# Optimization experiments

Hardware: AMD Instinct MI355X
Metric: run time of the kernel (lower is better)

## Reference

```python
import jax, jax.numpy as jnp
import numpy as np

N = 20000      # nodes / tokens
H = 256        # hidden_size
NH = 8         # num_heads
HD = NH * H    # num_heads * hidden_size = 2048
EPS = 1e-5


def setup_inputs() -> dict:
    key = jax.random.key(0)
    ks = jax.random.split(key, 24)

    def lin_w(k, i, o):
        # xavier-ish scale for a Linear weight stored as [in, out]
        return jax.random.normal(k, (i, o), jnp.float32) * (1.0 / np.sqrt(i))

    inp = {
        'q': jax.random.normal(ks[0], (N, H), jnp.float32),
        'k': jax.random.normal(ks[1], (N, H), jnp.float32),
        'v': jax.random.normal(ks[2], (N, H), jnp.float32),
        'layer': 1,
        'Wq1': lin_w(ks[3], H, HD), 'bq1': jnp.zeros((HD,), jnp.float32),
        'Wk1': lin_w(ks[4], H, HD), 'bk1': jnp.zeros((HD,), jnp.float32),
        'Wq2': lin_w(ks[5], H, HD), 'bq2': jnp.zeros((HD,), jnp.float32),
        'Wk2': lin_w(ks[6], H, HD), 'bk2': jnp.zeros((HD,), jnp.float32),
        'Wv':  lin_w(ks[7], H, HD), 'bv':  jnp.zeros((HD,), jnp.float32),
        'ln_g': jnp.ones((HD,), jnp.float32),
        'ln_b': jnp.zeros((HD,), jnp.float32),
        'Wo': lin_w(ks[8], HD, H), 'bo': jnp.zeros((H,), jnp.float32),
        'lq1': jax.random.normal(ks[9], (H,), jnp.float32) * 0.1,
        'lk1': jax.random.normal(ks[10], (H,), jnp.float32) * 0.1,
        'lq2': jax.random.normal(ks[11], (H,), jnp.float32) * 0.1,
        'lk2': jax.random.normal(ks[12], (H,), jnp.float32) * 0.1,
    }
    return inp


def reference(q, k, v, layer, Wq1, bq1, Wk1, bk1, Wq2, bq2, Wk2, bk2,
              Wv, bv, ln_g, ln_b, Wo, bo, lq1, lk1, lq2, lk2):
    # projections: [N, H] -> [N, HD]
    q1 = q @ Wq1 + bq1
    k1 = k @ Wk1 + bk1
    q2 = q @ Wq2 + bq2
    k2 = k @ Wk2 + bk2
    vv = v @ Wv + bv

    # linear attention: K^T V -> [HD, HD]  (dropout is identity in eval mode)
    k1v = k1.T @ vv
    k2v = k2.T @ vv

    # lambda gating (scalars)
    lam1 = jnp.exp(jnp.sum(lq1 * lk1))
    lam2 = jnp.exp(jnp.sum(lq2 * lk2))
    lam_init = 0.8 - 0.6 * jnp.exp(jnp.asarray(-0.3 * layer, jnp.float32))
    lam_full = lam1 - lam2 + lam_init

    # Q @ (K^T V), differential subtraction: [N, HD]
    x = q1 @ k1v - lam_full * (q2 @ k2v)

    # LayerNorm over last dim (biased variance, eps=1e-5, like torch)
    mu = jnp.mean(x, axis=-1, keepdims=True)
    var = jnp.mean(jnp.square(x - mu), axis=-1, keepdims=True)
    x = (x - mu) / jnp.sqrt(var + EPS) * ln_g + ln_b

    x = x * (1.0 - lam_init)
    return x @ Wo + bo  # [N, H]
```

## Files before the change

kernel.cpp:

```cpp
#include <hip/hip_runtime.h>
#include <stdint.h>

typedef __bf16 bf16x8 __attribute__((ext_vector_type(8)));
typedef __bf16 bf16x4v __attribute__((ext_vector_type(4)));
typedef float f32x4 __attribute__((ext_vector_type(4)));
typedef float f32x2 __attribute__((ext_vector_type(2)));
typedef unsigned short u16x4 __attribute__((ext_vector_type(4)));
typedef unsigned short u16x8 __attribute__((ext_vector_type(8)));

#define NTOK 20000
#define HIW  256
#define HD   2048
#define LDK  66
#define BUFS 8448

static __device__ __forceinline__ float bf2f(unsigned short h) {
  union { unsigned u; float f; } c; c.u = ((unsigned)h) << 16;
  return c.f;
}
static __device__ __forceinline__ unsigned short fbits(float x) {
  __bf16 h = (__bf16)x;
  return __builtin_bit_cast(unsigned short, h);
}

#define WRED(x) { x += __shfl_xor(x,32); x += __shfl_xor(x,16); x += __shfl_xor(x,8); \
                  x += __shfl_xor(x,4);  x += __shfl_xor(x,2);  x += __shfl_xor(x,1); }


__global__ __launch_bounds__(512) void k_front(
    const float* __restrict__ kk, const float* __restrict__ vv,
    const float* __restrict__ Wq1, const float* __restrict__ Wk1,
    const float* __restrict__ Wq2, const float* __restrict__ Wk2,
    const float* __restrict__ lq1, const float* __restrict__ lk1,
    const float* __restrict__ lq2, const float* __restrict__ lk2,
    const float* __restrict__ bq1, const float* __restrict__ bk1,
    const float* __restrict__ bq2, const float* __restrict__ bk2,
    const int* __restrict__ layer,
    unsigned short* __restrict__ S_part, float* __restrict__ skp, float* __restrict__ svp,
    unsigned short* __restrict__ Pc_part, float* __restrict__ scal) {
  __shared__ unsigned short SH[4 * BUFS];
  const int b = blockIdx.x;
  const int t = threadIdx.x, lane = t & 63, wave = t >> 6;
  const int wr = (wave >> 1) * 32, wc = (wave & 1) * 64;
  const int r15 = lane & 15, kg = (lane >> 4) * 8;

  if (b < 256) {
    const int z = b & 63, by = (b >> 6) & 1, bx = (b >> 7) & 1;
    const int i0 = bx * 128, j0 = by * 128;
    const int n_lo = z * 313;
    const int cnt = (NTOK - n_lo < 313) ? (NTOK - n_lo) : 313;
    f32x4 acc[2][4];
    #pragma unroll
    for (int m = 0; m < 2; ++m)
      #pragma unroll
      for (int n = 0; n < 4; ++n) acc[m][n] = (f32x4){0.f, 0.f, 0.f, 0.f};

    const int matsel = t >> 8, col = t & 127, half = (t >> 7) & 1;
    const float* src = matsel ? vv : kk;
    const int gcol = (matsel ? j0 : i0) + col;
    unsigned short* Lb0 = SH + matsel * BUFS;
    const int tbase = half * 32;
    float csum = 0.f;
    float rA[32], rB[32];

#define LOADK(dst, KT)                                                        \
    { _Pragma("unroll")                                                       \
      for (int g = 0; g < 32; ++g) {                                          \
        int nn = (KT) * 64 + tbase + g;                                       \
        dst[g] = (nn < cnt) ? src[(size_t)(n_lo + nn) * HIW + gcol] : 0.f;    \
      } }
#define WRITEK(dstp, rr)                                                      \
    { _Pragma("unroll")                                                       \
      for (int g4 = 0; g4 < 8; ++g4) {                                        \
        bf16x4v o;                                                            \
        _Pragma("unroll")                                                     \
        for (int u = 0; u < 4; ++u) {                                         \
          float x = rr[g4 * 4 + u]; csum += x; o[u] = (__bf16)x;              \
        }                                                                     \
        *(bf16x4v*)&dstp[col * LDK + tbase + g4 * 4] = o;                     \
      } }

    LOADK(rA, 0)
    WRITEK(Lb0, rA)
    LOADK(rB, 1)
    asm volatile("s_waitcnt lgkmcnt(0)" ::: "memory");
    __builtin_amdgcn_s_barrier();

    #pragma unroll
    for (int kt = 0; kt < 5; ++kt) {
      const unsigned short* Akr = SH + (kt & 1) * 2 * BUFS;
      const unsigned short* Bkr = Akr + BUFS;
      __builtin_amdgcn_s_setprio(1);
      #pragma unroll
      for (int ks = 0; ks < 2; ++ks) {
        const int ko = ks * 32 + kg;
        bf16x8 ah[2], bh[4];
        #pragma unroll
        for (int m = 0; m < 2; ++m)
          ah[m] = *(const bf16x8*)&Akr[(wr + m * 16 + r15) * LDK + ko];
        #pragma unroll
        for (int n = 0; n < 4; ++n)
          bh[n] = *(const bf16x8*)&Bkr[(wc + n * 16 + r15) * LDK + ko];
        #pragma unroll
        for (int m = 0; m < 2; ++m)
          #pragma unroll
          for (int n = 0; n < 4; ++n)
            acc[m][n] = __builtin_amdgcn_mfma_f32_16x16x32_bf16(ah[m], bh[n], acc[m][n], 0, 0, 0);
      }
      __builtin_amdgcn_s_setprio(0);
      if (kt < 4) {
        unsigned short* Ld = SH + ((kt + 1) & 1) * 2 * BUFS + matsel * BUFS;
        if ((kt & 1) == 0) {
          WRITEK(Ld, rB)
          if (kt + 2 <= 4) LOADK(rA, kt + 2)
        } else {
          WRITEK(Ld, rA)
          if (kt + 2 <= 4) LOADK(rB, kt + 2)
        }
      }
      asm volatile("s_waitcnt lgkmcnt(0)" ::: "memory");
      __builtin_amdgcn_s_barrier();
    }
#undef LOADK
#undef WRITEK
    const int rg = (lane >> 4) * 4;
    unsigned short* Sp = S_part + (size_t)z * 65536;
    #pragma unroll
    for (int m = 0; m < 2; ++m)
      #pragma unroll
      for (int n = 0; n < 4; ++n)
        #pragma unroll
        for (int r = 0; r < 4; ++r)
          Sp[(i0 + wr + m * 16 + rg + r) * 256 + (j0 + wc + n * 16 + r15)] = fbits(acc[m][n][r]);
    if (bx == by) {
      float* red = (float*)SH;
      red[t] = csum;
      __syncthreads();
      if (t < 128)      skp[z * 256 + i0 + t]         = red[t] + red[t + 128];
      else if (t < 256) svp[z * 256 + j0 + (t - 128)] = red[t + 128] + red[t + 256];
    }
  } else if (b < 384) {
    const int idx = b - 256;
    const int pair = idx >> 6, rem = idx & 63;
    const int z = rem & 15, by = (rem >> 4) & 1, bx = (rem >> 5) & 1;
    const int i0 = bx * 128, j0 = by * 128;
    const float* Wa = pair ? Wq2 : Wq1;
    const float* Wb = pair ? Wk2 : Wk1;
    f32x4 acc[2][4];
    #pragma unroll
    for (int m = 0; m < 2; ++m)
      #pragma unroll
      for (int n = 0; n < 4; ++n) acc[m][n] = (f32x4){0.f, 0.f, 0.f, 0.f};
    unsigned short* Ak = SH;
    unsigned short* Bk = SH + BUFS;
    const int srow = t >> 2, sq = (t & 3) * 16;
    for (int kt = 0; kt < 2; ++kt) {
      const int kb = z * 128 + kt * 64 + sq;
      __syncthreads();
      #pragma unroll
      for (int c = 0; c < 4; ++c) {
        f32x4 a = *(const f32x4*)&Wa[(size_t)(i0 + srow) * HD + kb + c * 4];
        f32x4 bb = *(const f32x4*)&Wb[(size_t)(j0 + srow) * HD + kb + c * 4];
        bf16x4v oa, ob;
        #pragma unroll
        for (int u = 0; u < 4; ++u) { oa[u] = (__bf16)a[u]; ob[u] = (__bf16)bb[u]; }
        *(bf16x4v*)&Ak[srow * LDK + sq + c * 4] = oa;
        *(bf16x4v*)&Bk[srow * LDK + sq + c * 4] = ob;
      }
      __syncthreads();
      __builtin_amdgcn_s_setprio(1);
      #pragma unroll
      for (int ks = 0; ks < 2; ++ks) {
        const int ko = ks * 32 + kg;
        bf16x8 ah[2], bh[4];
        #pragma unroll
        for (int m = 0; m < 2; ++m)
          ah[m] = *(const bf16x8*)&Ak[(wr + m * 16 + r15) * LDK + ko];
        #pragma unroll
        for (int n = 0; n < 4; ++n)
          bh[n] = *(const bf16x8*)&Bk[(wc + n * 16 + r15) * LDK + ko];
        #pragma unroll
        for (int m = 0; m < 2; ++m)
          #pragma unroll
          for (int n = 0; n < 4; ++n)
            acc[m][n] = __builtin_amdgcn_mfma_f32_16x16x32_bf16(ah[m], bh[n], acc[m][n], 0, 0, 0);
      }
      __builtin_amdgcn_s_setprio(0);
    }
    const int rg = (lane >> 4) * 4;
    unsigned short* Pp = Pc_part + (size_t)(pair * 16 + z) * 65536;
    #pragma unroll
    for (int m = 0; m < 2; ++m)
      #pragma unroll
      for (int n = 0; n < 4; ++n)
        #pragma unroll
        for (int r = 0; r < 4; ++r)
          Pp[(i0 + wr + m * 16 + rg + r) * 256 + (j0 + wc + n * 16 + r15)] = fbits(acc[m][n][r]);
  } else {
    float* red = (float*)SH;
    if (t < 256) {
      float p1 = lq1[t] * lk1[t], p2 = lq2[t] * lk2[t];
      float d1 = 0.f, d2 = 0.f;
      #pragma unroll
      for (int u = 0; u < 8; ++u) {
        d1 += bq1[t * 8 + u] * bk1[t * 8 + u];
        d2 += bq2[t * 8 + u] * bk2[t * 8 + u];
      }
      WRED(p1); WRED(p2); WRED(d1); WRED(d2);
      int w = t >> 6;
      if ((t & 63) == 0) { red[w] = p1; red[4 + w] = p2; red[8 + w] = d1; red[12 + w] = d2; }
    }
    __syncthreads();
    if (t == 0) {
      float s1 = red[0] + red[1] + red[2] + red[3];
      float s2 = red[4] + red[5] + red[6] + red[7];
      float dd1 = red[8] + red[9] + red[10] + red[11];
      float dd2 = red[12] + red[13] + red[14] + red[15];
      float li = 0.8f - 0.6f * expf(-0.3f * (float)layer[0]);
      float lam = expf(s1) - expf(s2) + li;
      scal[0] = lam; scal[1] = -lam; scal[2] = 1.0f - li; scal[3] = li;
      scal[4] = dd1 - lam * dd2;
    }
  }
}

__global__ __launch_bounds__(256) void k_sred(
    const unsigned short* __restrict__ S_part, const unsigned short* __restrict__ Pc_part,
    const float* __restrict__ skp, const float* __restrict__ svp,
    float* __restrict__ S, float* __restrict__ Pc,
    float* __restrict__ sk, float* __restrict__ sv,
    const float* __restrict__ Wk1, const float* __restrict__ Wk2,
    const float* __restrict__ Wq1, const float* __restrict__ Wq2,
    const float* __restrict__ bq1, const float* __restrict__ bq2,
    const float* __restrict__ bk1, const float* __restrict__ bk2,
    const float* __restrict__ scal, float* __restrict__ gc, float* __restrict__ uc) {
  int b = blockIdx.x, t = threadIdx.x;
  if (b < 64) {
    size_t idx = (size_t)b * 1024 + t * 4;
    f32x4 s = {0.f, 0.f, 0.f, 0.f};
    #pragma unroll 4
    for (int z = 0; z < 64; ++z) {
      u16x4 h = *(const u16x4*)&S_part[(size_t)z * 65536 + idx];
      #pragma unroll
      for (int u = 0; u < 4; ++u) s[u] += bf2f(h[u]);
    }
    *(f32x4*)&S[idx] = s;
  } else if (b < 96) {
    size_t idx = (size_t)(b - 64) * 2048 + t * 8;
    float s1[8] = {}, s2[8] = {};
    #pragma unroll 2
    for (int z = 0; z < 16; ++z) {
      u16x8 ha = *(const u16x8*)&Pc_part[(size_t)z * 65536 + idx];
      u16x8 hb = *(const u16x8*)&Pc_part[(size_t)(16 + z) * 65536 + idx];
      #pragma unroll
      for (int u = 0; u < 8; ++u) { s1[u] += bf2f(ha[u]); s2[u] += bf2f(hb[u]); }
    }
    float lam = scal[0];
    #pragma unroll
    for (int u = 0; u < 8; ++u) Pc[idx + u] = s1[u] - lam * s2[u];
  } else if (b < 98) {
    const float* src = (b == 96) ? skp : svp;
    float s = 0.f;
    for (int z = 0; z < 64; ++z) s += src[z * 256 + t];
    if (b == 96) sk[t] = s; else sv[t] = s;
  } else {
    int bb = b - 98, lane = t & 63, w = t >> 6;
    bool dogc = bb < 16;
    const float* A1 = dogc ? Wk1 : Wq1;
    const float* A2 = dogc ? Wk2 : Wq2;
    const float* x1 = dogc ? bq1 : bk1;
    const float* x2 = dogc ? bq2 : bk2;
    float* outv = dogc ? gc : uc;
    float lam = scal[0];
    int rb = (bb & 15) * 16 + w * 4;
    for (int q2 = 0; q2 < 4; ++q2) {
      int row = rb + q2;
      float s1 = 0.f, s2 = 0.f;
      #pragma unroll
      for (int c = 0; c < 8; ++c) {
        int kk2 = c * 256 + lane * 4;
        f32x4 a1 = *(const f32x4*)&A1[(size_t)row * HD + kk2];
        f32x4 a2 = *(const f32x4*)&A2[(size_t)row * HD + kk2];
        f32x4 v1 = *(const f32x4*)&x1[kk2];
        f32x4 v2 = *(const f32x4*)&x2[kk2];
        #pragma unroll
        for (int u = 0; u < 4; ++u) { s1 += a1[u] * v1[u]; s2 += a2[u] * v2[u]; }
      }
      WRED(s1); WRED(s2);
      if (lane == 0) outv[row] = s1 - lam * s2;
    }
  }
}

__global__ __launch_bounds__(256) void k_ac(
    const float* __restrict__ Pc, const float* __restrict__ S,
    const float* __restrict__ gc, const float* __restrict__ sk,
    float* __restrict__ Ac, float* __restrict__ tc, float* __restrict__ rv,
    float* __restrict__ scal) {
  int b = blockIdx.x, t = threadIdx.x;
  if (b < 32) {
    __shared__ float Pt[32][68];
    __shared__ float St[64][68];
    int i0 = (b >> 2) * 32, j0 = (b & 3) * 64;
    int ti = t >> 5, tj = t & 31;
    float acc[4][2] = {};
    for (int kt = 0; kt < 256; kt += 64) {
      __syncthreads();
      {
        int rr = t >> 3, c8 = (t & 7) * 8;
        *(f32x4*)&Pt[rr][c8] = *(const f32x4*)&Pc[(i0 + rr) * 256 + kt + c8];
        *(f32x4*)&Pt[rr][c8 + 4] = *(const f32x4*)&Pc[(i0 + rr) * 256 + kt + c8 + 4];
      }
      {
        int rr = t >> 2, c16 = (t & 3) * 16;
        #pragma unroll
        for (int c = 0; c < 4; ++c)
          *(f32x4*)&St[rr][c16 + c * 4] = *(const f32x4*)&S[(kt + rr) * 256 + j0 + c16 + c * 4];
      }
      __syncthreads();
      #pragma unroll 8
      for (int k2 = 0; k2 < 64; ++k2) {
        float a[4];
        #pragma unroll
        for (int u = 0; u < 4; ++u) a[u] = Pt[ti * 4 + u][k2];
        f32x2 b2 = *(const f32x2*)&St[k2][tj * 2];
        #pragma unroll
        for (int u = 0; u < 4; ++u) { acc[u][0] += a[u] * b2[0]; acc[u][1] += a[u] * b2[1]; }
      }
    }
    #pragma unroll
    for (int u = 0; u < 4; ++u) {
      Ac[(i0 + ti * 4 + u) * 256 + j0 + tj * 2] = acc[u][0];
      Ac[(i0 + ti * 4 + u) * 256 + j0 + tj * 2 + 1] = acc[u][1];
    }
  } else if (b == 32) {
    int lane = t & 63, w = t >> 6;
    f32x4 sk4 = *(const f32x4*)&sk[lane * 4];
    for (int ii = 0; ii < 64; ++ii) {
      int i = w * 64 + ii;
      f32x4 p4 = *(const f32x4*)&Pc[i * 256 + lane * 4];
      float s = p4[0] * sk4[0] + p4[1] * sk4[1] + p4[2] * sk4[2] + p4[3] * sk4[3];
      WRED(s);
      if (lane == 0) tc[i] = s;
    }
  } else {
    float s0 = 0.f, s1 = 0.f, s2 = 0.f, s3 = 0.f;
    #pragma unroll 4
    for (int i = 0; i < 256; i += 4) {
      s0 += gc[i] * S[i * 256 + t];
      s1 += gc[i + 1] * S[(i + 1) * 256 + t];
      s2 += gc[i + 2] * S[(i + 2) * 256 + t];
      s3 += gc[i + 3] * S[(i + 3) * 256 + t];
    }
    rv[t] = (s0 + s1) + (s2 + s3);
    if (t < 64) {
      f32x4 g4 = *(const f32x4*)&gc[t * 4];
      f32x4 sk4 = *(const f32x4*)&sk[t * 4];
      float a = g4[0] * sk4[0] + g4[1] * sk4[1] + g4[2] * sk4[2] + g4[3] * sk4[3];
      WRED(a);
      if (t == 0) scal[5] = a;
    }
  }
}

__global__ __launch_bounds__(256) void k_gc(
    const float* __restrict__ Ac, const float* __restrict__ Wv,
    const float* __restrict__ tc, const float* __restrict__ uc,
    const float* __restrict__ sv, const float* __restrict__ rv,
    const float* __restrict__ bv, const float* __restrict__ scal,
    float* __restrict__ Gc, float* __restrict__ cc) {
  __shared__ float At[64][68];
  __shared__ float Bt[64][132];
  __shared__ float svr[256], rvr[256];
  int t = threadIdx.x;
  int i0 = blockIdx.x * 64, j0 = blockIdx.y * 128;
  int ti = t >> 5, tj = t & 31;
  svr[t] = sv[t]; rvr[t] = rv[t];
  float acc[8][4] = {};
  f32x4 swa = {0.f, 0.f, 0.f, 0.f}, sca = {0.f, 0.f, 0.f, 0.f};
  for (int kt = 0; kt < 256; kt += 64) {
    __syncthreads();
    {
      int rr = t >> 2, c16 = (t & 3) * 16;
      #pragma unroll
      for (int c = 0; c < 4; ++c)
        *(f32x4*)&At[rr][c16 + c * 4] = *(const f32x4*)&Ac[(i0 + rr) * 256 + kt + c16 + c * 4];
    }
    {
      int rr = t >> 2, c32 = (t & 3) * 32;
      #pragma unroll
      for (int c = 0; c < 8; ++c)
        *(f32x4*)&Bt[rr][c32 + c * 4] = *(const f32x4*)&Wv[(size_t)(kt + rr) * HD + j0 + c32 + c * 4];
    }
    __syncthreads();
    #pragma unroll 8
    for (int k2 = 0; k2 < 64; ++k2) {
      float a[8];
      #pragma unroll
      for (int u = 0; u < 8; ++u) a[u] = At[ti * 8 + u][k2];
      f32x4 b = *(const f32x4*)&Bt[k2][tj * 4];
      float svk = svr[kt + k2], rvk = rvr[kt + k2];
      swa += b * svk; sca += b * rvk;
      #pragma unroll
      for (int u = 0; u < 8; ++u)
        #pragma unroll
        for (int v = 0; v < 4; ++v) acc[u][v] += a[u] * b[v];
    }
  }
  int j = j0 + tj * 4;
  f32x4 bv4 = *(const f32x4*)&bv[j];
  f32x4 wnb;
  #pragma unroll
  for (int v = 0; v < 4; ++v) wnb[v] = swa[v] + 20000.0f * bv4[v];
  if (blockIdx.x == 0 && ti == 0) {
    float ac = scal[5], dc = scal[4];
    f32x4 ccv;
    #pragma unroll
    for (int v = 0; v < 4; ++v) ccv[v] = sca[v] + ac * bv4[v] + dc * wnb[v];
    *(f32x4*)&cc[j] = ccv;
  }
  #pragma unroll
  for (int u = 0; u < 8; ++u) {
    int i = i0 + ti * 8 + u;
    float tci = tc[i], uci = uc[i];
    f32x4 o;
    #pragma unroll
    for (int v = 0; v < 4; ++v)
      o[v] = acc[u][v] + tci * bv4[v] + uci * wnb[v];
    *(f32x4*)&Gc[(size_t)i * HD + j] = o;
  }
}

__global__ __launch_bounds__(256) void k_post(
    const float* __restrict__ Gc, const float* __restrict__ cc,
    const float* __restrict__ Wo, const float* __restrict__ g,
    const float* __restrict__ lnb, const float* __restrict__ scal_c,
    unsigned short* __restrict__ Bt2, float* __restrict__ M_part,
    float* __restrict__ Hc_part, float* __restrict__ scal) {
  __shared__ float SMEM[8768];
  int b = blockIdx.x, t = threadIdx.x;
  if (b < 17) {
    int lane = t & 63, w = t >> 6;
    if (b < 16) {
      int rb = b * 16 + w * 4;
      for (int q2 = 0; q2 < 4; ++q2) {
        int row = rb + q2;
        float s1 = 0.f, s2 = 0.f;
        #pragma unroll
        for (int c = 0; c < 8; ++c) {
          int kk2 = c * 256 + lane * 4;
          f32x4 g4 = *(const f32x4*)&Gc[(size_t)row * HD + kk2];
          f32x4 c4v = *(const f32x4*)&cc[kk2];
          #pragma unroll
          for (int u = 0; u < 4; ++u) { s1 += g4[u]; s2 += g4[u] * c4v[u]; }
        }
        WRED(s1); WRED(s2);
        if (lane == 0) {
          int base = ((256 + (row >> 5)) * 64 + ((row >> 3) & 3) * 16) * 8 + (row & 7);
          Bt2[base] = fbits(s1 * (1.0f / 2048.0f));
          Bt2[base + 8] = fbits(s2);
        }
      }
    } else {
      float s1 = 0.f, s2 = 0.f;
      #pragma unroll
      for (int c = 0; c < 2; ++c) {
        f32x4 v = *(const f32x4*)&cc[t * 8 + c * 4];
        #pragma unroll
        for (int u = 0; u < 4; ++u) { s1 += v[u]; s2 += v[u] * v[u]; }
      }
      WRED(s1); WRED(s2);
      if ((t & 63) == 0) { SMEM[t >> 6] = s1; SMEM[4 + (t >> 6)] = s2; }
      __syncthreads();
      if (t == 0) {
        scal[6] = SMEM[4] + SMEM[5] + SMEM[6] + SMEM[7];
        scal[7] = (SMEM[0] + SMEM[1] + SMEM[2] + SMEM[3]) * (1.0f / 2048.0f);
      }
      for (int idx = t; idx < 14 * 256; idx += 256) {
        int ci = idx >> 8, kk2 = idx & 255;
        int col = 514 + ci;
        Bt2[((256 + (kk2 >> 5)) * 64 + ((kk2 >> 3) & 3) * 16 + (col & 15)) * 8 + (kk2 & 7)] = 0;
      }
    }
  } else if (b < 81) {
    float (*Gi)[68] = (float(*)[68])SMEM;
    float (*Gj)[69] = (float(*)[69])(SMEM + 64 * 68);
    int idx = b - 17;
    int bx = idx & 3, by = (idx >> 2) & 3, z = idx >> 4;
    int i0 = bx * 64, j0 = by * 64;
    int ti = t >> 5, tj = t & 31;
    float acc[8][2] = {};
    for (int kt = 0; kt < 512; kt += 64) {
      int kb = z * 512 + kt;
      __syncthreads();
      {
        int rr = t >> 2, c16 = (t & 3) * 16;
        #pragma unroll
        for (int c = 0; c < 4; ++c) {
          *(f32x4*)&Gi[rr][c16 + c * 4] = *(const f32x4*)&Gc[(size_t)(i0 + rr) * HD + kb + c16 + c * 4];
          *(f32x4*)&Gj[rr][c16 + c * 4] = *(const f32x4*)&Gc[(size_t)(j0 + rr) * HD + kb + c16 + c * 4];
        }
      }
      __syncthreads();
      #pragma unroll 8
      for (int k2 = 0; k2 < 64; ++k2) {
        float a[8];
        #pragma unroll
        for (int u = 0; u < 8; ++u) a[u] = Gi[ti * 8 + u][k2];
        float b0 = Gj[tj * 2][k2], b1 = Gj[tj * 2 + 1][k2];
        #pragma unroll
        for (int u = 0; u < 8; ++u) { acc[u][0] += a[u] * b0; acc[u][1] += a[u] * b1; }
      }
    }
    #pragma unroll
    for (int u = 0; u < 8; ++u) {
      M_part[(size_t)z * 65536 + (i0 + ti * 8 + u) * 256 + j0 + tj * 2] = acc[u][0];
      M_part[(size_t)z * 65536 + (i0 + ti * 8 + u) * 256 + j0 + tj * 2 + 1] = acc[u][1];
    }
  } else {
    float (*At)[68] = (float(*)[68])SMEM;
    float (*Bt)[68] = (float(*)[68])(SMEM + 32 * 68);
    int idx = b - 81;
    int bx = idx % 9, rem = idx / 9, by = rem & 3, z = rem >> 2;
    int i0 = bx * 32, j0 = by * 64;
    float s2 = scal_c[2];
    int ti = t >> 5, tj = t & 31;
    float acc[4][2] = {};
    for (int kt = 0; kt < 512; kt += 64) {
      int kb = z * 512 + kt;
      __syncthreads();
      {
        int rr = t >> 3, c8 = (t & 7) * 8, gi = i0 + rr;
        #pragma unroll
        for (int h = 0; h < 8; h += 4) {
          f32x4 g4 = *(const f32x4*)&g[kb + c8 + h];
          f32x4 a;
          if (gi < 256) {
            f32x4 gg = *(const f32x4*)&Gc[(size_t)gi * HD + kb + c8 + h];
            #pragma unroll
            for (int u = 0; u < 4; ++u) a[u] = gg[u] * g4[u];
          } else if (gi == 256) {
            a = g4;
          } else if (gi == 257) {
            f32x4 c4v = *(const f32x4*)&cc[kb + c8 + h];
            #pragma unroll
            for (int u = 0; u < 4; ++u) a[u] = c4v[u] * g4[u];
          } else if (gi == 258) {
            a = *(const f32x4*)&lnb[kb + c8 + h];
          } else {
            a = (f32x4){0.f, 0.f, 0.f, 0.f};
          }
          *(f32x4*)&At[rr][c8 + h] = a;
        }
      }
      {
        int rr = t >> 2, c16 = (t & 3) * 16;
        #pragma unroll
        for (int c = 0; c < 4; ++c) {
          f32x4 bb = *(const f32x4*)&Wo[(size_t)(kb + rr) * 256 + j0 + c16 + c * 4];
          #pragma unroll
          for (int u = 0; u < 4; ++u) bb[u] *= s2;
          *(f32x4*)&Bt[rr][c16 + c * 4] = bb;
        }
      }
      __syncthreads();
      #pragma unroll 8
      for (int k2 = 0; k2 < 64; ++k2) {
        float a[4];
        #pragma unroll
        for (int u = 0; u < 4; ++u) a[u] = At[ti * 4 + u][k2];
        f32x2 b2 = *(const f32x2*)&Bt[k2][tj * 2];
        #pragma unroll
        for (int u = 0; u < 4; ++u) { acc[u][0] += a[u] * b2[0]; acc[u][1] += a[u] * b2[1]; }
      }
    }
    #pragma unroll
    for (int u = 0; u < 4; ++u) {
      Hc_part[(size_t)z * 73728 + (i0 + ti * 4 + u) * 256 + j0 + tj * 2] = acc[u][0];
      Hc_part[(size_t)z * 73728 + (i0 + ti * 4 + u) * 256 + j0 + tj * 2 + 1] = acc[u][1];
    }
  }
}

__global__ __launch_bounds__(256) void k_red2(
    const float* __restrict__ M_part, const float* __restrict__ Hc_part,
    const float* __restrict__ bo, unsigned short* __restrict__ Bt2,
    float* __restrict__ wbar, float* __restrict__ hcv, float* __restrict__ bcv) {
  int bi = blockIdx.x, z2 = blockIdx.y, t = threadIdx.x;
  if (z2 == 2) {
    if (bi != 0) return;
    float s0 = 0.f, s1 = 0.f, s2 = 0.f;
    #pragma unroll
    for (int z = 0; z < 4; ++z) {
      s0 += Hc_part[(size_t)z * 73728 + 256 * 256 + t];
      s1 += Hc_part[(size_t)z * 73728 + 257 * 256 + t];
      s2 += Hc_part[(size_t)z * 73728 + 258 * 256 + t];
    }
    wbar[t] = s0; hcv[t] = s1; bcv[t] = s2 + bo[t];
    return;
  }
  __shared__ unsigned short T[64][256];
  const float* src = z2 ? Hc_part : M_part;
  const size_t sp = z2 ? 73728 : 65536;
  const int base = z2 ? 256 : 0;
  for (int ii = 0; ii < 64; ++ii) {
    int i = bi * 64 + ii;
    float s = 0.f;
    #pragma unroll
    for (int z = 0; z < 4; ++z) s += src[z * sp + i * 256 + t];
    T[ii][t] = fbits(s);
  }
  __syncthreads();
  const int col = base + t;
  #pragma unroll
  for (int c = 0; c < 64; c += 8) {
    u16x8 o;
    #pragma unroll
    for (int u = 0; u < 8; ++u) o[u] = T[c + u][t];
    int kk0 = bi * 64 + c;
    int addr = (((col >> 4) * 8 + (kk0 >> 5)) * 64 + ((kk0 >> 3) & 3) * 16 + (col & 15)) * 8;
    *(u16x8*)&Bt2[addr] = o;
  }
}

__global__ __launch_bounds__(256) void k_out(
    const float* __restrict__ q, const unsigned short* __restrict__ Bt2,
    const float* __restrict__ hcv, const float* __restrict__ wbar,
    const float* __restrict__ bcv, const float* __restrict__ scal,
    float* __restrict__ out) {
  __shared__ unsigned short As[32 * 264];
  __shared__ float sqp[2][32];
  __shared__ float muL[32], m2L[32];
  const int t = threadIdx.x, lane = t & 63, wave = t >> 6;
  const int row0 = blockIdx.x * 32;
  const int r15 = lane & 15, kg = lane >> 4;
  {
    int r = t >> 3;
    #pragma unroll
    for (int ci = 0; ci < 8; ++ci) {
      int col = ci * 32 + (t & 7) * 4;
      f32x4 v = *(const f32x4*)&q[(size_t)(row0 + r) * HIW + col];
      bf16x4v o;
      #pragma unroll
      for (int u = 0; u < 4; ++u) o[u] = (__bf16)v[u];
      *(bf16x4v*)&As[r * 264 + col] = o;
    }
  }
  __syncthreads();
  const int wc = wave * 128;
  const unsigned short* bbase = Bt2 + (size_t)(wave * 8) * 4096 + (size_t)lane * 8;
  f32x4 acc[2][9];
  #pragma unroll
  for (int m = 0; m < 2; ++m)
    #pragma unroll
    for (int n = 0; n < 9; ++n) acc[m][n] = (f32x4){0.f, 0.f, 0.f, 0.f};
  __builtin_amdgcn_s_setprio(1);
  #pragma unroll
  for (int ko = 0; ko < 8; ++ko) {
    bf16x8 af0 = *(const bf16x8*)&As[r15 * 264 + ko * 32 + kg * 8];
    bf16x8 af1 = *(const bf16x8*)&As[(16 + r15) * 264 + ko * 32 + kg * 8];
    #pragma unroll
    for (int ni = 0; ni < 9; ++ni) {
      if (ni == 8 && wave != 3) continue;
      bf16x8 bfr = *(const bf16x8*)&bbase[ni * 4096 + ko * 512];
      acc[0][ni] = __builtin_amdgcn_mfma_f32_16x16x32_bf16(af0, bfr, acc[0][ni], 0, 0, 0);
      acc[1][ni] = __builtin_amdgcn_mfma_f32_16x16x32_bf16(af1, bfr, acc[1][ni], 0, 0, 0);
    }
  }
  __builtin_amdgcn_s_setprio(0);
  if (wave < 2) {
    #pragma unroll
    for (int m = 0; m < 2; ++m)
      #pragma unroll
      for (int r = 0; r < 4; ++r) {
        int rowl = m * 16 + kg * 4 + r;
        float p = 0.f;
        #pragma unroll
        for (int ni = 0; ni < 8; ++ni) {
          int col = wc + ni * 16 + r15;
          p += acc[m][ni][r] * bf2f(As[rowl * 264 + col]);
        }
        p += __shfl_xor(p, 1); p += __shfl_xor(p, 2);
        p += __shfl_xor(p, 4); p += __shfl_xor(p, 8);
        if (r15 == 0) sqp[wave][rowl] = p;
      }
  }
  if (wave == 3) {
    #pragma unroll
    for (int m = 0; m < 2; ++m)
      #pragma unroll
      for (int r = 0; r < 4; ++r) {
        int rowl = m * 16 + kg * 4 + r;
        if (r15 == 0) muL[rowl] = acc[m][8][r];
        if (r15 == 1) m2L[rowl] = acc[m][8][r];
      }
  }
  __syncthreads();
  if (wave >= 2) {
    const float css = scal[6], cbar = scal[7];
    #pragma unroll
    for (int m = 0; m < 2; ++m)
      #pragma unroll
      for (int r = 0; r < 4; ++r) {
        int rowl = m * 16 + kg * 4 + r;
        float mu = muL[rowl] + cbar;
        float ss = sqp[0][rowl] + sqp[1][rowl] + 2.0f * m2L[rowl] + css;
        float var = ss * (1.0f / 2048.0f) - mu * mu;
        float rstd = rsqrtf(var + 1e-5f);
        int grow = row0 + rowl;
        #pragma unroll
        for (int ni = 0; ni < 8; ++ni) {
          int oc = (wc - 256) + ni * 16 + r15;
          float zv = acc[m][ni][r] + hcv[oc];
          out[(size_t)grow * HIW + oc] = rstd * (zv - mu * wbar[oc]) + bcv[oc];
        }
      }
  }
}

extern "C" void kernel_launch(void* const* d_in, const int* in_sizes, int n_in,
                              void* d_out, int out_size, void* d_ws, size_t ws_size,
                              hipStream_t stream) {
  const float* q   = (const float*)d_in[0];
  const float* k   = (const float*)d_in[1];
  const float* v   = (const float*)d_in[2];
  const int* layer = (const int*)d_in[3];
  const float* Wq1 = (const float*)d_in[4];  const float* bq1 = (const float*)d_in[5];
  const float* Wk1 = (const float*)d_in[6];  const float* bk1 = (const float*)d_in[7];
  const float* Wq2 = (const float*)d_in[8];  const float* bq2 = (const float*)d_in[9];
  const float* Wk2 = (const float*)d_in[10]; const float* bk2 = (const float*)d_in[11];
  const float* Wv  = (const float*)d_in[12]; const float* bv  = (const float*)d_in[13];
  const float* lng = (const float*)d_in[14]; const float* lnb = (const float*)d_in[15];
  const float* Wo  = (const float*)d_in[16]; const float* bo  = (const float*)d_in[17];
  const float* lq1 = (const float*)d_in[18]; const float* lk1 = (const float*)d_in[19];
  const float* lq2 = (const float*)d_in[20]; const float* lk2 = (const float*)d_in[21];

  char* p = (char*)d_ws;
  unsigned short* S_part = (unsigned short*)p;  p += (size_t)64 * 65536 * 2;
  float* skp = (float*)p;     p += 64 * 256 * 4;
  float* svp = (float*)p;     p += 64 * 256 * 4;
  unsigned short* Pc_part = (unsigned short*)p; p += (size_t)32 * 65536 * 2;
  float* S  = (float*)p;      p += 65536 * 4;
  float* Pc = (float*)p;      p += 65536 * 4;
  float* sk = (float*)p;      p += 1024;
  float* sv = (float*)p;      p += 1024;
  float* gc = (float*)p;      p += 1024;
  float* uc = (float*)p;      p += 1024;
  float* tc = (float*)p;      p += 1024;
  float* rv = (float*)p;      p += 1024;
  float* cc  = (float*)p;     p += 2048 * 4;
  float* Ac  = (float*)p;     p += 65536 * 4;
  float* Gc  = (float*)p;     p += (size_t)2048 * 256 * 4;
  float* M_part  = (float*)p; p += (size_t)4 * 65536 * 4;
  float* Hc_part = (float*)p; p += (size_t)4 * 288 * 256 * 4;
  unsigned short* Bt2 = (unsigned short*)p; p += (size_t)135168 * 2;
  float* wbar = (float*)p;    p += 1024;
  float* hcv  = (float*)p;    p += 1024;
  float* bcv  = (float*)p;    p += 1024;
  float* scal = (float*)p;    p += 256;

  const dim3 b256(256);
  k_front<<<dim3(385), dim3(512), 0, stream>>>(k, v, Wq1, Wk1, Wq2, Wk2,
      lq1, lk1, lq2, lk2, bq1, bk1, bq2, bk2, layer, S_part, skp, svp, Pc_part, scal);
  k_sred<<<dim3(130), b256, 0, stream>>>(S_part, Pc_part, skp, svp, S, Pc, sk, sv,
                                         Wk1, Wk2, Wq1, Wq2, bq1, bq2, bk1, bk2, scal, gc, uc);
  k_ac<<<dim3(34), b256, 0, stream>>>(Pc, S, gc, sk, Ac, tc, rv, scal);
  k_gc<<<dim3(4, 16), b256, 0, stream>>>(Ac, Wv, tc, uc, sv, rv, bv, scal, Gc, cc);
  k_post<<<dim3(225), b256, 0, stream>>>(Gc, cc, Wo, lng, lnb, scal, Bt2, M_part, Hc_part, scal);
  k_red2<<<dim3(4, 3), b256, 0, stream>>>(M_part, Hc_part, bo, Bt2, wbar, hcv, bcv);
  k_out<<<dim3(625), b256, 0, stream>>>(q, Bt2, hcv, wbar, bcv, scal, (float*)d_out);
}
```

Measured before the change: 184.5 us.

## Pre-transpose K and V to bf16 and compute K^T V from transposed tiles

The front kernel now converts k and v to bf16 and writes them transposed (token-contiguous per feature) along with per-tile column sums. The S = K^T V product moves into a new mid kernel that streams these transposed tiles with wide vector loads and accumulates into S with float atomics, replacing the bf16 partial buffers and their reduction pass. The W-product blocks are retiled to 4x4 MFMA fragments per wave. The aim is to replace the strided per-element fp32 reads of k and v with coalesced loads and to drop the S_part reduction. The cost is an extra round trip through a transposed workspace, a memset, atomics whose order is not fixed, and workspace aliasing with later buffers.

```diff
diff --git a/kernel.cpp b/kernel.cpp
--- a/kernel.cpp
+++ b/kernel.cpp
@@ -9,10 +9,11 @@
 typedef unsigned short u16x8 __attribute__((ext_vector_type(8)));
 
 #define NTOK 20000
+#define NTP  20480
 #define HIW  256
 #define HD   2048
-#define LDK  66
-#define BUFS 8448
+#define LDKP 66
+#define LDS2 72
 
 static __device__ __forceinline__ float bf2f(unsigned short h) {
   union { unsigned u; float f; } c; c.u = ((unsigned)h) << 16;
@@ -27,7 +28,7 @@
                   x += __shfl_xor(x,4);  x += __shfl_xor(x,2);  x += __shfl_xor(x,1); }
 
 
-__global__ __launch_bounds__(512) void k_front(
+__global__ __launch_bounds__(256) void k_front(
     const float* __restrict__ kk, const float* __restrict__ vv,
     const float* __restrict__ Wq1, const float* __restrict__ Wk1,
     const float* __restrict__ Wq2, const float* __restrict__ Wk2,
@@ -36,180 +37,110 @@
     const float* __restrict__ bq1, const float* __restrict__ bk1,
     const float* __restrict__ bq2, const float* __restrict__ bk2,
     const int* __restrict__ layer,
-    unsigned short* __restrict__ S_part, float* __restrict__ skp, float* __restrict__ svp,
+    unsigned short* __restrict__ kT, unsigned short* __restrict__ vT,
+    float* __restrict__ skp, float* __restrict__ svp,
     unsigned short* __restrict__ Pc_part, float* __restrict__ scal) {
-  __shared__ unsigned short SH[4 * BUFS];
-  const int b = blockIdx.x;
-  const int t = threadIdx.x, lane = t & 63, wave = t >> 6;
-  const int wr = (wave >> 1) * 32, wc = (wave & 1) * 64;
-  const int r15 = lane & 15, kg = (lane >> 4) * 8;
-
-  if (b < 256) {
-    const int z = b & 63, by = (b >> 6) & 1, bx = (b >> 7) & 1;
+  __shared__ float SMEM[64][260];
+  const int b = blockIdx.x, t = threadIdx.x;
+
+  if (b < 640) {
+    const int tile = b >> 1, m = b & 1;
+    const float* src = m ? vv : kk;
+    unsigned short* dstT = m ? vT : kT;
+    float* sump = m ? svp : skp;
+    #pragma unroll
+    for (int i = 0; i < 16; ++i) {
+      int ch = i * 256 + t;
+      int row = ch >> 6, c4 = (ch & 63) * 4;
+      int gtok = tile * 64 + row;
+      f32x4 val = {0.f, 0.f, 0.f, 0.f};
+      if (gtok < NTOK) val = *(const f32x4*)&src[(size_t)gtok * HIW + c4];
+      *(f32x4*)&SMEM[row][c4] = val;
+    }
+    __syncthreads();
+    float sum = 0.f;
+    unsigned short cv[64];
+    #pragma unroll
+    for (int tok = 0; tok < 64; ++tok) {
+      float x = SMEM[tok][t];
+      sum += x;
+      cv[tok] = fbits(x);
+    }
+    sump[tile * 256 + t] = sum;
+    size_t base = (size_t)t * NTP + tile * 64;
+    #pragma unroll
+    for (int s = 0; s < 8; ++s)
+      *(u16x8*)&dstT[base + s * 8] = *(const u16x8*)&cv[s * 8];
+  } else if (b < 768) {
+    unsigned short* Ak = (unsigned short*)SMEM;
+    unsigned short* Bk = Ak + 128 * LDKP;
+    const int idx = b - 640;
+    const int pair = idx >> 6, rem = idx & 63;
+    const int z = rem & 15, by = (rem >> 4) & 1, bx = (rem >> 5) & 1;
     const int i0 = bx * 128, j0 = by * 128;
-    const int n_lo = z * 313;
-    const int cnt = (NTOK - n_lo < 313) ? (NTOK - n_lo) : 313;
-    f32x4 acc[2][4];
-    #pragma unroll
-    for (int m = 0; m < 2; ++m)
+    const int lane = t & 63, wave = t >> 6;
+    const int wr = (wave >> 1) * 64, wc = (wave & 1) * 64;
+    const int r15 = lane & 15, kg = (lane >> 4) * 8;
+    const float* Wa = pair ? Wq2 : Wq1;
+    const float* Wb = pair ? Wk2 : Wk1;
+    f32x4 acc[4][4];
+    #pragma unroll
+    for (int m = 0; m < 4; ++m)
       #pragma unroll
       for (int n = 0; n < 4; ++n) acc[m][n] = (f32x4){0.f, 0.f, 0.f, 0.f};
-
-    const int matsel = t >> 8, col = t & 127, half = (t >> 7) & 1;
-    const float* src = matsel ? vv : kk;
-    const int gcol = (matsel ? j0 : i0) + col;
-    unsigned short* Lb0 = SH + matsel * BUFS;
-    const int tbase = half * 32;
-    float csum = 0.f;
-    float rA[32], rB[32];
-
-#define LOADK(dst, KT)                                                        \
-    { _Pragma("unroll")                                                       \
-      for (int g = 0; g < 32; ++g) {                                          \
-        int nn = (KT) * 64 + tbase + g;                                       \
-        dst[g] = (nn < cnt) ? src[(size_t)(n_lo + nn) * HIW + gcol] : 0.f;    \
-      } }
-#define WRITEK(dstp, rr)                                                      \
-    { _Pragma("unroll")                                                       \
-      for (int g4 = 0; g4 < 8; ++g4) {                                        \
-        bf16x4v o;                                                            \
-        _Pragma("unroll")                                                     \
-        for (int u = 0; u < 4; ++u) {                                         \
-          float x = rr[g4 * 4 + u]; csum += x; o[u] = (__bf16)x;              \
-        }                                                                     \
-        *(bf16x4v*)&dstp[col * LDK + tbase + g4 * 4] = o;                     \
-      } }
-
-    LOADK(rA, 0)
-    WRITEK(Lb0, rA)
-    LOADK(rB, 1)
-    asm volatile("s_waitcnt lgkmcnt(0)" ::: "memory");
-    __builtin_amdgcn_s_barrier();
-
-    #pragma unroll
-    for (int kt = 0; kt < 5; ++kt) {
-      const unsigned short* Akr = SH + (kt & 1) * 2 * BUFS;
-      const unsigned short* Bkr = Akr + BUFS;
-      __builtin_amdgcn_s_setprio(1);
+    const int srow = t >> 1, sh = (t & 1) * 32;
+    for (int kt = 0; kt < 2; ++kt) {
+      const int kb = z * 128 + kt * 64 + sh;
+      __syncthreads();
+      #pragma unroll
+      for (int c = 0; c < 8; ++c) {
+        f32x4 a = *(const f32x4*)&Wa[(size_t)(i0 + srow) * HD + kb + c * 4];
+        f32x4 bb = *(const f32x4*)&Wb[(size_t)(j0 + srow) * HD + kb + c * 4];
+        bf16x4v oa, ob;
+        #pragma unroll
+        for (int u = 0; u < 4; ++u) { oa[u] = (__bf16)a[u]; ob[u] = (__bf16)bb[u]; }
+        *(bf16x4v*)&Ak[srow * LDKP + sh + c * 4] = oa;
+        *(bf16x4v*)&Bk[srow * LDKP + sh + c * 4] = ob;
+      }
+      __syncthreads();
       #pragma unroll
       for (int ks = 0; ks < 2; ++ks) {
         const int ko = ks * 32 + kg;
-        bf16x8 ah[2], bh[4];
-        #pragma unroll
-        for (int m = 0; m < 2; ++m)
-          ah[m] = *(const bf16x8*)&Akr[(wr + m * 16 + r15) * LDK + ko];
+        bf16x8 ah[4], bh[4];
+        #pragma unroll
+        for (int m = 0; m < 4; ++m)
+          ah[m] = *(const bf16x8*)&Ak[(wr + m * 16 + r15) * LDKP + ko];
         #pragma unroll
         for (int n = 0; n < 4; ++n)
-          bh[n] = *(const bf16x8*)&Bkr[(wc + n * 16 + r15) * LDK + ko];
-        #pragma unroll
-        for (int m = 0; m < 2; ++m)
+          bh[n] = *(const bf16x8*)&Bk[(wc + n * 16 + r15) * LDKP + ko];
+        #pragma unroll
+        for (int m = 0; m < 4; ++m)
           #pragma unroll
           for (int n = 0; n < 4; ++n)
             acc[m][n] = __builtin_amdgcn_mfma_f32_16x16x32_bf16(ah[m], bh[n], acc[m][n], 0, 0, 0);
       }
-      __builtin_amdgcn_s_setprio(0);
-      if (kt < 4) {
-        unsigned short* Ld = SH + ((kt + 1) & 1) * 2 * BUFS + matsel * BUFS;
-        if ((kt & 1) == 0) {
-          WRITEK(Ld, rB)
-          if (kt + 2 <= 4) LOADK(rA, kt + 2)
-        } else {
-          WRITEK(Ld, rA)
-          if (kt + 2 <= 4) LOADK(rB, kt + 2)
-        }
-      }
-      asm volatile("s_waitcnt lgkmcnt(0)" ::: "memory");
-      __builtin_amdgcn_s_barrier();
-    }
-#undef LOADK
-#undef WRITEK
-    const int rg = (lane >> 4) * 4;
-    unsigned short* Sp = S_part + (size_t)z * 65536;
-    #pragma unroll
-    for (int m = 0; m < 2; ++m)
-      #pragma unroll
-      for (int n = 0; n < 4; ++n)
-        #pragma unroll
-        for (int r = 0; r < 4; ++r)
-          Sp[(i0 + wr + m * 16 + rg + r) * 256 + (j0 + wc + n * 16 + r15)] = fbits(acc[m][n][r]);
-    if (bx == by) {
-      float* red = (float*)SH;
-      red[t] = csum;
-      __syncthreads();
-      if (t < 128)      skp[z * 256 + i0 + t]         = red[t] + red[t + 128];
-      else if (t < 256) svp[z * 256 + j0 + (t - 128)] = red[t + 128] + red[t + 256];
-    }
-  } else if (b < 384) {
-    const int idx = b - 256;
-    const int pair = idx >> 6, rem = idx & 63;
-    const int z = rem & 15, by = (rem >> 4) & 1, bx = (rem >> 5) & 1;
-    const int i0 = bx * 128, j0 = by * 128;
-    const float* Wa = pair ? Wq2 : Wq1;
-    const float* Wb = pair ? Wk2 : Wk1;
-    f32x4 acc[2][4];
-    #pragma unroll
-    for (int m = 0; m < 2; ++m)
-      #pragma unroll
-      for (int n = 0; n < 4; ++n) acc[m][n] = (f32x4){0.f, 0.f, 0.f, 0.f};
-    unsigned short* Ak = SH;
-    unsigned short* Bk = SH + BUFS;
-    const int srow = t >> 2, sq = (t & 3) * 16;
-    for (int kt = 0; kt < 2; ++kt) {
-      const int kb = z * 128 + kt * 64 + sq;
-      __syncthreads();
-      #pragma unroll
-      for (int c = 0; c < 4; ++c) {
-        f32x4 a = *(const f32x4*)&Wa[(size_t)(i0 + srow) * HD + kb + c * 4];
-        f32x4 bb = *(const f32x4*)&Wb[(size_t)(j0 + srow) * HD + kb + c * 4];
-        bf16x4v oa, ob;
-        #pragma unroll
-        for (int u = 0; u < 4; ++u) { oa[u] = (__bf16)a[u]; ob[u] = (__bf16)bb[u]; }
-        *(bf16x4v*)&Ak[srow * LDK + sq + c * 4] = oa;
-        *(bf16x4v*)&Bk[srow * LDK + sq + c * 4] = ob;
-      }
-      __syncthreads();
-      __builtin_amdgcn_s_setprio(1);
-      #pragma unroll
-      for (int ks = 0; ks < 2; ++ks) {
-        const int ko = ks * 32 + kg;
-        bf16x8 ah[2], bh[4];
-        #pragma unroll
-        for (int m = 0; m < 2; ++m)
-          ah[m] = *(const bf16x8*)&Ak[(wr + m * 16 + r15) * LDK + ko];
-        #pragma unroll
-        for (int n = 0; n < 4; ++n)
-          bh[n] = *(const bf16x8*)&Bk[(wc + n * 16 + r15) * LDK + ko];
-        #pragma unroll
-        for (int m = 0; m < 2; ++m)
-          #pragma unroll
-          for (int n = 0; n < 4; ++n)
-            acc[m][n] = __builtin_amdgcn_mfma_f32_16x16x32_bf16(ah[m], bh[n], acc[m][n], 0, 0, 0);
-      }
-      __builtin_amdgcn_s_setprio(0);
     }
     const int rg = (lane >> 4) * 4;
     unsigned short* Pp = Pc_part + (size_t)(pair * 16 + z) * 65536;
     #pragma unroll
-    for (int m = 0; m < 2; ++m)
+    for (int m = 0; m < 4; ++m)
       #pragma unroll
       for (int n = 0; n < 4; ++n)
         #pragma unroll
         for (int r = 0; r < 4; ++r)
           Pp[(i0 + wr + m * 16 + rg + r) * 256 + (j0 + wc + n * 16 + r15)] = fbits(acc[m][n][r]);
   } else {
-    float* red = (float*)SH;
-    if (t < 256) {
-      float p1 = lq1[t] * lk1[t], p2 = lq2[t] * lk2[t];
-      float d1 = 0.f, d2 = 0.f;
-      #pragma unroll
-      for (int u = 0; u < 8; ++u) {
-        d1 += bq1[t * 8 + u] * bk1[t * 8 + u];
-        d2 += bq2[t * 8 + u] * bk2[t * 8 + u];
-      }
-      WRED(p1); WRED(p2); WRED(d1); WRED(d2);
-      int w = t >> 6;
-      if ((t & 63) == 0) { red[w] = p1; red[4 + w] = p2; red[8 + w] = d1; red[12 + w] = d2; }
-    }
+    float* red = (float*)SMEM;
+    float p1 = lq1[t] * lk1[t], p2 = lq2[t] * lk2[t];
+    float d1 = 0.f, d2 = 0.f;
+    #pragma unroll
+    for (int u = 0; u < 8; ++u) {
+      d1 += bq1[t * 8 + u] * bk1[t * 8 + u];
+      d2 += bq2[t * 8 + u] * bk2[t * 8 + u];
+    }
+    WRED(p1); WRED(p2); WRED(d1); WRED(d2);
+    int w = t >> 6;
+    if ((t & 63) == 0) { red[w] = p1; red[4 + w] = p2; red[8 + w] = d1; red[12 + w] = d2; }
     __syncthreads();
     if (t == 0) {
       float s1 = red[0] + red[1] + red[2] + red[3];
@@ -224,70 +155,150 @@
   }
 }
 
-__global__ __launch_bounds__(256) void k_sred(
-    const unsigned short* __restrict__ S_part, const unsigned short* __restrict__ Pc_part,
+__global__ __launch_bounds__(512) void k_mid(
+    const unsigned short* __restrict__ kT, const unsigned short* __restrict__ vT,
+    float* __restrict__ S, const unsigned short* __restrict__ Pc_part,
     const float* __restrict__ skp, const float* __restrict__ svp,
-    float* __restrict__ S, float* __restrict__ Pc,
-    float* __restrict__ sk, float* __restrict__ sv,
+    float* __restrict__ Pc, float* __restrict__ sk, float* __restrict__ sv,
     const float* __restrict__ Wk1, const float* __restrict__ Wk2,
     const float* __restrict__ Wq1, const float* __restrict__ Wq2,
     const float* __restrict__ bq1, const float* __restrict__ bq2,
     const float* __restrict__ bk1, const float* __restrict__ bk2,
     const float* __restrict__ scal, float* __restrict__ gc, float* __restrict__ uc) {
-  int b = blockIdx.x, t = threadIdx.x;
-  if (b < 64) {
-    size_t idx = (size_t)b * 1024 + t * 4;
-    f32x4 s = {0.f, 0.f, 0.f, 0.f};
-    #pragma unroll 4
-    for (int z = 0; z < 64; ++z) {
-      u16x4 h = *(const u16x4*)&S_part[(size_t)z * 65536 + idx];
-      #pragma unroll
-      for (int u = 0; u < 4; ++u) s[u] += bf2f(h[u]);
-    }
-    *(f32x4*)&S[idx] = s;
-  } else if (b < 96) {
-    size_t idx = (size_t)(b - 64) * 2048 + t * 8;
-    float s1[8] = {}, s2[8] = {};
-    #pragma unroll 2
-    for (int z = 0; z < 16; ++z) {
-      u16x8 ha = *(const u16x8*)&Pc_part[(size_t)z * 65536 + idx];
-      u16x8 hb = *(const u16x8*)&Pc_part[(size_t)(16 + z) * 65536 + idx];
-      #pragma unroll
-      for (int u = 0; u < 8; ++u) { s1[u] += bf2f(ha[u]); s2[u] += bf2f(hb[u]); }
-    }
-    float lam = scal[0];
-    #pragma unroll
-    for (int u = 0; u < 8; ++u) Pc[idx + u] = s1[u] - lam * s2[u];
-  } else if (b < 98) {
-    const float* src = (b == 96) ? skp : svp;
-    float s = 0.f;
-    for (int z = 0; z < 64; ++z) s += src[z * 256 + t];
-    if (b == 96) sk[t] = s; else sv[t] = s;
+  __shared__ unsigned short SB[2 * 2 * 128 * LDS2];
+  const int b = blockIdx.x, t = threadIdx.x;
+
+  if (b < 256) {
+    const int z = b & 63, by = (b >> 6) & 1, bx = (b >> 7) & 1;
+    const int i0 = bx * 128, j0 = by * 128;
+    const int tok0 = z * 320;
+    const int lane = t & 63, wave = t >> 6;
+    const int wr = (wave >> 1) * 32, wc = (wave & 1) * 64;
+    const int r15 = lane & 15, kg = (lane >> 4) * 8;
+    const int m = t >> 8;
+    const int local = t & 255;
+    const int row2 = local >> 1;
+    const int koff = (local & 1) * 32;
+    const unsigned short* srcT = m ? vT : kT;
+    const size_t rbase = (size_t)((m ? j0 : i0) + row2) * NTP + tok0 + koff;
+    const int lds_off = m * 128 * LDS2 + row2 * LDS2 + koff;
+
+    f32x4 acc[2][4];
+    #pragma unroll
+    for (int mm = 0; mm < 2; ++mm)
+      #pragma unroll
+      for (int n = 0; n < 4; ++n) acc[mm][n] = (f32x4){0.f, 0.f, 0.f, 0.f};
+    u16x8 rA[4], rB[4];
+
+#define LOADT(R, KT)                                                          \
+    { _Pragma("unroll")                                                       \
+      for (int c = 0; c < 4; ++c)                                             \
+        R[c] = *(const u16x8*)&srcT[rbase + (KT) * 64 + c * 8]; }
+#define WRITET(BUF, R)                                                        \
+    { unsigned short* d = &SB[(BUF) * 2 * 128 * LDS2 + lds_off];              \
+      _Pragma("unroll")                                                       \
+      for (int c = 0; c < 4; ++c) *(u16x8*)&d[c * 8] = R[c]; }
+
+    LOADT(rA, 0)
+    WRITET(0, rA)
+    LOADT(rB, 1)
+    asm volatile("s_waitcnt lgkmcnt(0)" ::: "memory");
+    __builtin_amdgcn_s_barrier();
+
+    #pragma unroll
+    for (int kt = 0; kt < 5; ++kt) {
+      const unsigned short* Ab = &SB[(kt & 1) * 2 * 128 * LDS2];
+      const unsigned short* Bb = Ab + 128 * LDS2;
+      __builtin_amdgcn_s_setprio(1);
+      #pragma unroll
+      for (int ks = 0; ks < 2; ++ks) {
+        const int ko = ks * 32 + kg;
+        bf16x8 ah[2], bh[4];
+        #pragma unroll
+        for (int mm = 0; mm < 2; ++mm)
+          ah[mm] = *(const bf16x8*)&Ab[(wr + mm * 16 + r15) * LDS2 + ko];
+        #pragma unroll
+        for (int n = 0; n < 4; ++n)
+          bh[n] = *(const bf16x8*)&Bb[(wc + n * 16 + r15) * LDS2 + ko];
+        #pragma unroll
+        for (int mm = 0; mm < 2; ++mm)
+          #pragma unroll
+          for (int n = 0; n < 4; ++n)
+            acc[mm][n] = __builtin_amdgcn_mfma_f32_16x16x32_bf16(ah[mm], bh[n], acc[mm][n], 0, 0, 0);
+      }
+      __builtin_amdgcn_s_setprio(0);
+      if (kt < 4) {
+        if ((kt & 1) == 0) {
+          WRITET(1, rB)
+          if (kt + 2 <= 4) LOADT(rA, kt + 2)
+        } else {
+          WRITET(0, rA)
+          if (kt + 2 <= 4) LOADT(rB, kt + 2)
+        }
+      }
+      asm volatile("s_waitcnt lgkmcnt(0)" ::: "memory");
+      __builtin_amdgcn_s_barrier();
+    }
+#undef LOADT
+#undef WRITET
+    const int rg = (lane >> 4) * 4;
+    #pragma unroll
+    for (int mm = 0; mm < 2; ++mm)
+      #pragma unroll
+      for (int n = 0; n < 4; ++n)
+        #pragma unroll
+        for (int r = 0; r < 4; ++r)
+          atomicAdd(&S[(i0 + wr + mm * 16 + rg + r) * 256 + (j0 + wc + n * 16 + r15)],
+                    acc[mm][n][r]);
+  } else if (b < 288) {
+    if (t < 256) {
+      size_t idx = (size_t)(b - 256) * 2048 + t * 8;
+      float s1[8] = {}, s2[8] = {};
+      #pragma unroll 2
+      for (int z = 0; z < 16; ++z) {
+        u16x8 ha = *(const u16x8*)&Pc_part[(size_t)z * 65536 + idx];
+        u16x8 hb = *(const u16x8*)&Pc_part[(size_t)(16 + z) * 65536 + idx];
+        #pragma unroll
+        for (int u = 0; u < 8; ++u) { s1[u] += bf2f(ha[u]); s2[u] += bf2f(hb[u]); }
+      }
+      float lam = scal[0];
+      #pragma unroll
+      for (int u = 0; u < 8; ++u) Pc[idx + u] = s1[u] - lam * s2[u];
+    }
+  } else if (b < 290) {
+    if (t < 256) {
+      const float* src = (b == 288) ? skp : svp;
+      float s = 0.f;
+      for (int z = 0; z < 320; ++z) s += src[z * 256 + t];
+      if (b == 288) sk[t] = s; else sv[t] = s;
+    }
   } else {
-    int bb = b - 98, lane = t & 63, w = t >> 6;
-    bool dogc = bb < 16;
-    const float* A1 = dogc ? Wk1 : Wq1;
-    const float* A2 = dogc ? Wk2 : Wq2;
-    const float* x1 = dogc ? bq1 : bk1;
-    const float* x2 = dogc ? bq2 : bk2;
-    float* outv = dogc ? gc : uc;
-    float lam = scal[0];
-    int rb = (bb & 15) * 16 + w * 4;
-    for (int q2 = 0; q2 < 4; ++q2) {
-      int row = rb + q2;
-      float s1 = 0.f, s2 = 0.f;
-      #pragma unroll
-      for (int c = 0; c < 8; ++c) {
-        int kk2 = c * 256 + lane * 4;
-        f32x4 a1 = *(const f32x4*)&A1[(size_t)row * HD + kk2];
-        f32x4 a2 = *(const f32x4*)&A2[(size_t)row * HD + kk2];
-        f32x4 v1 = *(const f32x4*)&x1[kk2];
-        f32x4 v2 = *(const f32x4*)&x2[kk2];
-        #pragma unroll
-        for (int u = 0; u < 4; ++u) { s1 += a1[u] * v1[u]; s2 += a2[u] * v2[u]; }
-      }
-      WRED(s1); WRED(s2);
-      if (lane == 0) outv[row] = s1 - lam * s2;
+    if (t < 256) {
+      int bb = b - 290, lane = t & 63, w = t >> 6;
+      bool dogc = bb < 16;
+      const float* A1 = dogc ? Wk1 : Wq1;
+      const float* A2 = dogc ? Wk2 : Wq2;
+      const float* x1 = dogc ? bq1 : bk1;
+      const float* x2 = dogc ? bq2 : bk2;
+      float* outv = dogc ? gc : uc;
+      float lam = scal[0];
+      int rb = (bb & 15) * 16 + w * 4;
+      for (int q2 = 0; q2 < 4; ++q2) {
+        int row = rb + q2;
+        float s1 = 0.f, s2 = 0.f;
+        #pragma unroll
+        for (int c = 0; c < 8; ++c) {
+          int kk2 = c * 256 + lane * 4;
+          f32x4 a1 = *(const f32x4*)&A1[(size_t)row * HD + kk2];
+          f32x4 a2 = *(const f32x4*)&A2[(size_t)row * HD + kk2];
+          f32x4 v1 = *(const f32x4*)&x1[kk2];
+          f32x4 v2 = *(const f32x4*)&x2[kk2];
+          #pragma unroll
+          for (int u = 0; u < 4; ++u) { s1 += a1[u] * v1[u]; s2 += a2[u] * v2[u]; }
+        }
+        WRED(s1); WRED(s2);
+        if (lane == 0) outv[row] = s1 - lam * s2;
+      }
     }
   }
 }
@@ -736,9 +747,16 @@
   const float* lq2 = (const float*)d_in[20]; const float* lk2 = (const float*)d_in[21];
 
   char* p = (char*)d_ws;
-  unsigned short* S_part = (unsigned short*)p;  p += (size_t)64 * 65536 * 2;
-  float* skp = (float*)p;     p += 64 * 256 * 4;
-  float* svp = (float*)p;     p += 64 * 256 * 4;
+  unsigned short* kT = (unsigned short*)p;
+  float* M_part  = (float*)p;
+  float* Hc_part = (float*)(p + 1048576);
+  unsigned short* Bt2 = (unsigned short*)(p + 1048576 + 1179648);
+  p += (size_t)256 * NTP * 2;
+  unsigned short* vT = (unsigned short*)p;
+  float* Gc = (float*)p;
+  p += (size_t)256 * NTP * 2;
+  float* skp = (float*)p;     p += (size_t)320 * 256 * 4;
+  float* svp = (float*)p;     p += (size_t)320 * 256 * 4;
   unsigned short* Pc_part = (unsigned short*)p; p += (size_t)32 * 65536 * 2;
   float* S  = (float*)p;      p += 65536 * 4;
   float* Pc = (float*)p;      p += 65536 * 4;
@@ -748,22 +766,19 @@
   float* uc = (float*)p;      p += 1024;
   float* tc = (float*)p;      p += 1024;
   float* rv = (float*)p;      p += 1024;
-  float* cc  = (float*)p;     p += 2048 * 4;
-  float* Ac  = (float*)p;     p += 65536 * 4;
-  float* Gc  = (float*)p;     p += (size_t)2048 * 256 * 4;
-  float* M_part  = (float*)p; p += (size_t)4 * 65536 * 4;
-  float* Hc_part = (float*)p; p += (size_t)4 * 288 * 256 * 4;
-  unsigned short* Bt2 = (unsigned short*)p; p += (size_t)135168 * 2;
+  float* cc = (float*)p;      p += 2048 * 4;
+  float* Ac = (float*)p;      p += 65536 * 4;
   float* wbar = (float*)p;    p += 1024;
   float* hcv  = (float*)p;    p += 1024;
   float* bcv  = (float*)p;    p += 1024;
   float* scal = (float*)p;    p += 256;
 
   const dim3 b256(256);
-  k_front<<<dim3(385), dim3(512), 0, stream>>>(k, v, Wq1, Wk1, Wq2, Wk2,
-      lq1, lk1, lq2, lk2, bq1, bk1, bq2, bk2, layer, S_part, skp, svp, Pc_part, scal);
-  k_sred<<<dim3(130), b256, 0, stream>>>(S_part, Pc_part, skp, svp, S, Pc, sk, sv,
-                                         Wk1, Wk2, Wq1, Wq2, bq1, bq2, bk1, bk2, scal, gc, uc);
+  hipMemsetAsync(S, 0, 65536 * 4, stream);
+  k_front<<<dim3(769), b256, 0, stream>>>(k, v, Wq1, Wk1, Wq2, Wk2,
+      lq1, lk1, lq2, lk2, bq1, bk1, bq2, bk2, layer, kT, vT, skp, svp, Pc_part, scal);
+  k_mid<<<dim3(322), dim3(512), 0, stream>>>(kT, vT, S, Pc_part, skp, svp, Pc, sk, sv,
+      Wk1, Wk2, Wq1, Wq2, bq1, bq2, bk1, bk2, scal, gc, uc);
   k_ac<<<dim3(34), b256, 0, stream>>>(Pc, S, gc, sk, Ac, tc, rv, scal);
   k_gc<<<dim3(4, 16), b256, 0, stream>>>(Ac, Wv, tc, uc, sv, rv, bv, scal, Gc, cc);
   k_post<<<dim3(225), b256, 0, stream>>>(Gc, cc, Wo, lng, lnb, scal, Bt2, M_part, Hc_part, scal);
```

After: 193.8 us. +5.0%, slower.
